# Optimization experiments

Measured on AMD Instinct MI355X. Metric: run time of the kernel, lower is better.

Reference implementation:

```python
import jax, jax.numpy as jnp
import numpy as np

NUM_HEADS = 8

def _proj(x, W, b):
    # 1x1 conv == channel-wise linear: x [B,Ci,H,W], W [Co,Ci], b [Co]
    return jnp.einsum('oi,bihw->bohw', W, x) + b[None, :, None, None]

def setup_inputs() -> dict:
    key = jax.random.key(0)
    ks = jax.random.split(key, 8)
    B, Cin, Cout, H, W = 4, 256, 256, 48, 48
    s = 1.0 / np.sqrt(Cin).astype(np.float32)
    return {
        'queries': jax.random.normal(ks[0], (B, Cin, H, W), jnp.float32),
        'keys':    jax.random.normal(ks[1], (B, Cin, H, W), jnp.float32),
        'values':  jax.random.normal(ks[2], (B, Cin, H, W), jnp.float32),
        'Wq': jax.random.normal(ks[3], (Cout, Cin), jnp.float32) * s,
        'bq': jnp.zeros((Cout,), jnp.float32),
        'Wk': jax.random.normal(ks[4], (Cout, Cin), jnp.float32) * s,
        'bk': jnp.zeros((Cout,), jnp.float32),
        'Wv': jax.random.normal(ks[5], (Cout, Cin), jnp.float32) * s,
        'bv': jnp.zeros((Cout,), jnp.float32),
        'Wo': jax.random.normal(ks[6], (Cout, Cout), jnp.float32) * s,
        'bo': jnp.zeros((Cout,), jnp.float32),
    }

def reference(queries, keys, values, Wq, bq, Wk, bk, Wv, bv, Wo, bo):
    B, _, H, W = values.shape
    Cout = Wq.shape[0]
    d = Cout // NUM_HEADS
    # project and split heads: [B, heads, d, N]
    q = _proj(queries, Wq, bq).reshape(B, NUM_HEADS, d, H * W)
    k = _proj(keys,    Wk, bk).reshape(B, NUM_HEADS, d, H * W)
    v = _proj(values,  Wv, bv).reshape(B, NUM_HEADS, d, H * W)
    scale = 1.0 / np.sqrt(Cout).astype(np.float32)  # source scales by sqrt(out_channels)
    attn = jax.nn.softmax(jnp.einsum('bhdn,bhdm->bhnm', q, k) * scale, axis=-1)
    out = jnp.einsum('bhdm,bhnm->bhdn', v, attn).reshape(B, Cout, H, W)
    return _proj(out, Wo, bo)
```

## Files before the change

### kernel.cpp

```cpp
#include <hip/hip_runtime.h>
#include <hip/hip_bf16.h>

#define NTOT 2304
#define CIN  256
#define DHEAD 32

typedef float  f32x4  __attribute__((ext_vector_type(4)));
typedef __bf16 bf16x8 __attribute__((ext_vector_type(8)));
typedef unsigned short u16x8 __attribute__((ext_vector_type(8)));

static __device__ __forceinline__ unsigned short f2bf(float f) {
    unsigned int u = __float_as_uint(f);
    u += 0x7fff + ((u >> 16) & 1);
    return (unsigned short)(u >> 16);
}

static __device__ __forceinline__ unsigned int pk2(float a, float b) {
    unsigned int r;
    asm("v_cvt_pk_bf16_f32 %0, %1, %2" : "=v"(r) : "v"(a), "v"(b));
    return r;
}

union U8 { unsigned short s[8]; bf16x8 v; };
union PB { unsigned int u[4]; bf16x8 v; };

__global__ __launch_bounds__(256) void pack_weights_kernel(
    const float* __restrict__ Wq, const float* __restrict__ bq,
    const float* __restrict__ Wk, const float* __restrict__ Wv,
    const float* __restrict__ Wo,
    unsigned short* __restrict__ Wq_b, unsigned short* __restrict__ Wk_b,
    unsigned short* __restrict__ Wv_b, unsigned short* __restrict__ Wo_b,
    float* __restrict__ bq_s)
{
    const float SQ = 1.44269504088896340736f / 16.0f;
    int i = blockIdx.x * 256 + threadIdx.x;
    Wq_b[i] = f2bf(Wq[i] * SQ);
    Wk_b[i] = f2bf(Wk[i]);
    Wv_b[i] = f2bf(Wv[i]);
    Wo_b[i] = f2bf(Wo[i]);
    if (blockIdx.x == 0) bq_s[threadIdx.x] = bq[threadIdx.x] * SQ;
}

__global__ __launch_bounds__(256) void proj_all_kernel(
    const float* __restrict__ qx, const float* __restrict__ kx,
    const float* __restrict__ vx,
    const unsigned short* __restrict__ Wqb, const unsigned short* __restrict__ Wkb,
    const unsigned short* __restrict__ Wvb,
    const float* __restrict__ bqs, const float* __restrict__ bk,
    const float* __restrict__ bv,
    unsigned short* __restrict__ Qa, unsigned short* __restrict__ Ka,
    unsigned short* __restrict__ Vp)
{
    const int which = blockIdx.z >> 2;
    const int b     = blockIdx.z & 3;
    const float* x = (which == 0) ? qx : (which == 1) ? kx : vx;
    const unsigned short* Wb = (which == 0) ? Wqb : (which == 1) ? Wkb : Wvb;
    const float* bias = (which == 0) ? bqs : (which == 1) ? bk : bv;
    unsigned short* out = (which == 0) ? Qa : (which == 1) ? Ka : Vp;

    const int n0  = blockIdx.x * 64;
    const int co0 = blockIdx.y * 64;
    const int t = threadIdx.x;
    const int lane = t & 63, w = t >> 6;
    const int g = lane >> 4, l15 = lane & 15;
    const int n_off  = (w & 1) * 32;
    const int co_off = (w >> 1) * 32;

    f32x4 acc[2][2] = {};
    const float* xb = x + (size_t)b * CIN * NTOT;

    for (int ci0 = 0; ci0 < CIN; ci0 += 32) {
        bf16x8 aF[2], bF[2];
        #pragma unroll
        for (int rn = 0; rn < 2; rn++) {
            const float* xp = xb + (size_t)(ci0 + 8 * g) * NTOT + (n0 + n_off + 16 * rn + l15);
            U8 a;
            #pragma unroll
            for (int j = 0; j < 8; j++) a.s[j] = f2bf(xp[(size_t)j * NTOT]);
            aF[rn] = a.v;
        }
        #pragma unroll
        for (int rc = 0; rc < 2; rc++)
            bF[rc] = *reinterpret_cast<const bf16x8*>(
                Wb + (size_t)(co0 + co_off + 16 * rc + l15) * CIN + ci0 + 8 * g);
        #pragma unroll
        for (int rn = 0; rn < 2; rn++)
            #pragma unroll
            for (int rc = 0; rc < 2; rc++)
                acc[rn][rc] = __builtin_amdgcn_mfma_f32_16x16x32_bf16(aF[rn], bF[rc], acc[rn][rc], 0, 0, 0);
    }

    #pragma unroll
    for (int rn = 0; rn < 2; rn++)
    #pragma unroll
    for (int rc = 0; rc < 2; rc++) {
        int co = co0 + co_off + 16 * rc + l15;
        float bs = bias[co];
        int bh = b * 8 + (co >> 5);
        int dd = co & 31;
        int nb = n0 + n_off + 16 * rn + 4 * g;
        if (which == 2) {
            ushort4 v;
            v.x = f2bf(acc[rn][rc][0] + bs);
            v.y = f2bf(acc[rn][rc][1] + bs);
            v.z = f2bf(acc[rn][rc][2] + bs);
            v.w = f2bf(acc[rn][rc][3] + bs);
            int p32 = 8 * ((nb >> 2) & 3) + 4 * ((nb >> 4) & 1);
            *reinterpret_cast<ushort4*>(
                out + (size_t)bh * 73728 + (nb >> 5) * 1024 + dd * 32 + p32) = v;
        } else {
            #pragma unroll
            for (int reg = 0; reg < 4; reg++)
                out[((size_t)bh * NTOT + (nb + reg)) * DHEAD + dd] = f2bf(acc[rn][rc][reg] + bs);
        }
    }
}

__global__ __launch_bounds__(256) void attn_kernel(
    const unsigned short* __restrict__ Qa,
    const unsigned short* __restrict__ Ka,
    const unsigned short* __restrict__ Vp,
    unsigned short* __restrict__ Ot)
{
    __shared__ __align__(16) float olds_a[3][64][17];
    __shared__ __align__(16) float olds_b[3][64][17];
    __shared__ float plsum_a[3][64][3];
    __shared__ float plsum_b[3][64][3];
    __shared__ __align__(16) unsigned short tlds[32][40];
    const int f = blockIdx.x;
    const int c = f & 7;
    const int k = f >> 3;
    const int kq = k / 36;
    const int bh = 4 * c + kq;
    const int qt = k - kq * 36;
    const int b = bh >> 3, h = bh & 7;
    const int t = threadIdx.x;
    const int w = t >> 6, lane = t & 63;
    const int g = lane >> 4, l15 = lane & 15;
    const int n_w = qt * 64;
    const int kw0 = w * 576;

    const unsigned short* Kb  = Ka + (size_t)bh * NTOT * DHEAD + l15 * DHEAD + 8 * g;
    const unsigned short* Vb0 = Vp + (size_t)bh * 73728 + l15 * 32 + 8 * g;
    const unsigned short* Vb1 = Vb0 + 512;

    bf16x8 qBa[2], qBb[2];
    #pragma unroll
    for (int r = 0; r < 2; r++) {
        qBa[r] = *reinterpret_cast<const bf16x8*>(
            Qa + ((size_t)bh * NTOT + n_w + 16 * r + l15) * DHEAD + 8 * g);
        qBb[r] = *reinterpret_cast<const bf16x8*>(
            Qa + ((size_t)bh * NTOT + n_w + 32 + 16 * r + l15) * DHEAD + 8 * g);
    }

    f32x4 oacc_a[2][2] = {};
    f32x4 oacc_b[2][2] = {};
    float psum_a[2] = {0.f, 0.f};
    float psum_b[2] = {0.f, 0.f};
    const f32x4 z4 = {0.f, 0.f, 0.f, 0.f};

    bf16x8 kA[4], kN[4], vA[4], vN[4];
    #pragma unroll
    for (int mc = 0; mc < 4; mc++) {
        kA[mc] = *reinterpret_cast<const bf16x8*>(Kb + (size_t)(kw0 + 16 * mc) * DHEAD);
        kN[mc] = *reinterpret_cast<const bf16x8*>(Kb + (size_t)(kw0 + 64 + 16 * mc) * DHEAD);
    }
    vA[0] = *reinterpret_cast<const bf16x8*>(Vb0 + (size_t)kw0 * 32);
    vA[1] = *reinterpret_cast<const bf16x8*>(Vb0 + (size_t)kw0 * 32 + 1024);
    vA[2] = *reinterpret_cast<const bf16x8*>(Vb1 + (size_t)kw0 * 32);
    vA[3] = *reinterpret_cast<const bf16x8*>(Vb1 + (size_t)kw0 * 32 + 1024);
    vN[0] = *reinterpret_cast<const bf16x8*>(Vb0 + (size_t)(kw0 + 64) * 32);
    vN[1] = *reinterpret_cast<const bf16x8*>(Vb0 + (size_t)(kw0 + 64) * 32 + 1024);
    vN[2] = *reinterpret_cast<const bf16x8*>(Vb1 + (size_t)(kw0 + 64) * 32);
    vN[3] = *reinterpret_cast<const bf16x8*>(Vb1 + (size_t)(kw0 + 64) * 32 + 1024);

    for (int it = 0; it < 9; it++) {
        {
            f32x4 s[2][4];
            #pragma unroll
            for (int r = 0; r < 2; r++)
                #pragma unroll
                for (int mc = 0; mc < 4; mc++)
                    s[r][mc] = __builtin_amdgcn_mfma_f32_16x16x32_bf16(kA[mc], qBa[r], z4, 0, 0, 0);

            float p[2][4][4];
            #pragma unroll
            for (int r = 0; r < 2; r++) {
                #pragma unroll
                for (int mc = 0; mc < 4; mc++)
                    #pragma unroll
                    for (int reg = 0; reg < 4; reg++)
                        p[r][mc][reg] = __builtin_amdgcn_exp2f(s[r][mc][reg]);
                float t0 = (p[r][0][0] + p[r][0][1]) + (p[r][0][2] + p[r][0][3]);
                float t1 = (p[r][1][0] + p[r][1][1]) + (p[r][1][2] + p[r][1][3]);
                float t2 = (p[r][2][0] + p[r][2][1]) + (p[r][2][2] + p[r][2][3]);
                float t3 = (p[r][3][0] + p[r][3][1]) + (p[r][3][2] + p[r][3][3]);
                psum_a[r] += (t0 + t1) + (t2 + t3);
            }

            PB pb[2][2];
            #pragma unroll
            for (int r = 0; r < 2; r++)
                #pragma unroll
                for (int hh = 0; hh < 2; hh++) {
                    pb[r][hh].u[0] = pk2(p[r][2*hh][0],   p[r][2*hh][1]);
                    pb[r][hh].u[1] = pk2(p[r][2*hh][2],   p[r][2*hh][3]);
                    pb[r][hh].u[2] = pk2(p[r][2*hh+1][0], p[r][2*hh+1][1]);
                    pb[r][hh].u[3] = pk2(p[r][2*hh+1][2], p[r][2*hh+1][3]);
                }

            #pragma unroll
            for (int r = 0; r < 2; r++) {
                oacc_a[r][0] = __builtin_amdgcn_mfma_f32_16x16x32_bf16(vA[0], pb[r][0].v, oacc_a[r][0], 0, 0, 0);
                oacc_a[r][0] = __builtin_amdgcn_mfma_f32_16x16x32_bf16(vA[1], pb[r][1].v, oacc_a[r][0], 0, 0, 0);
                oacc_a[r][1] = __builtin_amdgcn_mfma_f32_16x16x32_bf16(vA[2], pb[r][0].v, oacc_a[r][1], 0, 0, 0);
                oacc_a[r][1] = __builtin_amdgcn_mfma_f32_16x16x32_bf16(vA[3], pb[r][1].v, oacc_a[r][1], 0, 0, 0);
            }
        }
        {
            f32x4 s[2][4];
            #pragma unroll
            for (int r = 0; r < 2; r++)
                #pragma unroll
                for (int mc = 0; mc < 4; mc++)
                    s[r][mc] = __builtin_amdgcn_mfma_f32_16x16x32_bf16(kA[mc], qBb[r], z4, 0, 0, 0);

            float p[2][4][4];
            #pragma unroll
            for (int r = 0; r < 2; r++) {
                #pragma unroll
                for (int mc = 0; mc < 4; mc++)
                    #pragma unroll
                    for (int reg = 0; reg < 4; reg++)
                        p[r][mc][reg] = __builtin_amdgcn_exp2f(s[r][mc][reg]);
                float t0 = (p[r][0][0] + p[r][0][1]) + (p[r][0][2] + p[r][0][3]);
                float t1 = (p[r][1][0] + p[r][1][1]) + (p[r][1][2] + p[r][1][3]);
                float t2 = (p[r][2][0] + p[r][2][1]) + (p[r][2][2] + p[r][2][3]);
                float t3 = (p[r][3][0] + p[r][3][1]) + (p[r][3][2] + p[r][3][3]);
                psum_b[r] += (t0 + t1) + (t2 + t3);
            }

            PB pb[2][2];
            #pragma unroll
            for (int r = 0; r < 2; r++)
                #pragma unroll
                for (int hh = 0; hh < 2; hh++) {
                    pb[r][hh].u[0] = pk2(p[r][2*hh][0],   p[r][2*hh][1]);
                    pb[r][hh].u[1] = pk2(p[r][2*hh][2],   p[r][2*hh][3]);
                    pb[r][hh].u[2] = pk2(p[r][2*hh+1][0], p[r][2*hh+1][1]);
                    pb[r][hh].u[3] = pk2(p[r][2*hh+1][2], p[r][2*hh+1][3]);
                }

            #pragma unroll
            for (int r = 0; r < 2; r++) {
                oacc_b[r][0] = __builtin_amdgcn_mfma_f32_16x16x32_bf16(vA[0], pb[r][0].v, oacc_b[r][0], 0, 0, 0);
                oacc_b[r][0] = __builtin_amdgcn_mfma_f32_16x16x32_bf16(vA[1], pb[r][1].v, oacc_b[r][0], 0, 0, 0);
                oacc_b[r][1] = __builtin_amdgcn_mfma_f32_16x16x32_bf16(vA[2], pb[r][0].v, oacc_b[r][1], 0, 0, 0);
                oacc_b[r][1] = __builtin_amdgcn_mfma_f32_16x16x32_bf16(vA[3], pb[r][1].v, oacc_b[r][1], 0, 0, 0);
            }
        }

        int m2 = kw0 + (it + 2) * 64;
        if (it >= 7) m2 = kw0;
        #pragma unroll
        for (int mc = 0; mc < 4; mc++) {
            kA[mc] = kN[mc];
            kN[mc] = *reinterpret_cast<const bf16x8*>(Kb + (size_t)(m2 + 16 * mc) * DHEAD);
        }
        vA[0] = vN[0]; vA[1] = vN[1]; vA[2] = vN[2]; vA[3] = vN[3];
        vN[0] = *reinterpret_cast<const bf16x8*>(Vb0 + (size_t)m2 * 32);
        vN[1] = *reinterpret_cast<const bf16x8*>(Vb0 + (size_t)m2 * 32 + 1024);
        vN[2] = *reinterpret_cast<const bf16x8*>(Vb1 + (size_t)m2 * 32);
        vN[3] = *reinterpret_cast<const bf16x8*>(Vb1 + (size_t)m2 * 32 + 1024);
    }

    if (w > 0) {
        #pragma unroll
        for (int r = 0; r < 2; r++)
            #pragma unroll
            for (int dc = 0; dc < 2; dc++) {
                *reinterpret_cast<f32x4*>(&olds_a[w - 1][lane][8 * r + 4 * dc]) = oacc_a[r][dc];
                *reinterpret_cast<f32x4*>(&olds_b[w - 1][lane][8 * r + 4 * dc]) = oacc_b[r][dc];
            }
        plsum_a[w - 1][lane][0] = psum_a[0];
        plsum_a[w - 1][lane][1] = psum_a[1];
        plsum_b[w - 1][lane][0] = psum_b[0];
        plsum_b[w - 1][lane][1] = psum_b[1];
    }
    __syncthreads();
    if (w == 0) {
        #pragma unroll
        for (int ww = 0; ww < 3; ww++) {
            #pragma unroll
            for (int r = 0; r < 2; r++)
                #pragma unroll
                for (int dc = 0; dc < 2; dc++)
                    oacc_a[r][dc] += *reinterpret_cast<const f32x4*>(&olds_a[ww][lane][8 * r + 4 * dc]);
            psum_a[0] += plsum_a[ww][lane][0];
            psum_a[1] += plsum_a[ww][lane][1];
        }
        float lra[2];
        #pragma unroll
        for (int r = 0; r < 2; r++) {
            float ps = psum_a[r];
            ps += __shfl_xor(ps, 16);
            ps += __shfl_xor(ps, 32);
            lra[r] = 1.0f / ps;
        }
        #pragma unroll
        for (int r = 0; r < 2; r++)
            #pragma unroll
            for (int dc = 0; dc < 2; dc++) {
                ushort4 v;
                v.x = f2bf(oacc_a[r][dc][0] * lra[r]);
                v.y = f2bf(oacc_a[r][dc][1] * lra[r]);
                v.z = f2bf(oacc_a[r][dc][2] * lra[r]);
                v.w = f2bf(oacc_a[r][dc][3] * lra[r]);
                *reinterpret_cast<ushort4*>(&tlds[16 * r + l15][16 * dc + 4 * g]) = v;
            }
        #pragma unroll
        for (int i = 0; i < 2; i++) {
            int row = 16 * i + (lane >> 2), seg = lane & 3;
            u16x8 val = *reinterpret_cast<const u16x8*>(&tlds[row][seg * 8]);
            *reinterpret_cast<u16x8*>(
                Ot + ((size_t)b * NTOT + n_w + row) * CIN + h * DHEAD + seg * 8) = val;
        }

        #pragma unroll
        for (int ww = 0; ww < 3; ww++) {
            #pragma unroll
            for (int r = 0; r < 2; r++)
                #pragma unroll
                for (int dc = 0; dc < 2; dc++)
                    oacc_b[r][dc] += *reinterpret_cast<const f32x4*>(&olds_b[ww][lane][8 * r + 4 * dc]);
            psum_b[0] += plsum_b[ww][lane][0];
            psum_b[1] += plsum_b[ww][lane][1];
        }
        float lrb[2];
        #pragma unroll
        for (int r = 0; r < 2; r++) {
            float ps = psum_b[r];
            ps += __shfl_xor(ps, 16);
            ps += __shfl_xor(ps, 32);
            lrb[r] = 1.0f / ps;
        }
        #pragma unroll
        for (int r = 0; r < 2; r++)
            #pragma unroll
            for (int dc = 0; dc < 2; dc++) {
                ushort4 v;
                v.x = f2bf(oacc_b[r][dc][0] * lrb[r]);
                v.y = f2bf(oacc_b[r][dc][1] * lrb[r]);
                v.z = f2bf(oacc_b[r][dc][2] * lrb[r]);
                v.w = f2bf(oacc_b[r][dc][3] * lrb[r]);
                *reinterpret_cast<ushort4*>(&tlds[16 * r + l15][16 * dc + 4 * g]) = v;
            }
        #pragma unroll
        for (int i = 0; i < 2; i++) {
            int row = 16 * i + (lane >> 2), seg = lane & 3;
            u16x8 val = *reinterpret_cast<const u16x8*>(&tlds[row][seg * 8]);
            *reinterpret_cast<u16x8*>(
                Ot + ((size_t)b * NTOT + n_w + 32 + row) * CIN + h * DHEAD + seg * 8) = val;
        }
    }
}

__global__ __launch_bounds__(256) void out_proj_kernel(
    const unsigned short* __restrict__ Ot,
    const unsigned short* __restrict__ Wob,
    const float* __restrict__ bo,
    float* __restrict__ out)
{
    const int b   = blockIdx.z;
    const int n0  = blockIdx.x * 64;
    const int co0 = blockIdx.y * 64;
    const int t = threadIdx.x;
    const int lane = t & 63, w = t >> 6;
    const int g = lane >> 4, l15 = lane & 15;
    const int n_off  = (w & 1) * 32;
    const int co_off = (w >> 1) * 32;

    f32x4 acc[2][2] = {};
    for (int ci0 = 0; ci0 < CIN; ci0 += 32) {
        bf16x8 aF[2], bF[2];
        #pragma unroll
        for (int rn = 0; rn < 2; rn++)
            aF[rn] = *reinterpret_cast<const bf16x8*>(
                Ot + ((size_t)b * NTOT + n0 + n_off + 16 * rn + l15) * CIN + ci0 + 8 * g);
        #pragma unroll
        for (int rc = 0; rc < 2; rc++)
            bF[rc] = *reinterpret_cast<const bf16x8*>(
                Wob + (size_t)(co0 + co_off + 16 * rc + l15) * CIN + ci0 + 8 * g);
        #pragma unroll
        for (int rn = 0; rn < 2; rn++)
            #pragma unroll
            for (int rc = 0; rc < 2; rc++)
                acc[rn][rc] = __builtin_amdgcn_mfma_f32_16x16x32_bf16(aF[rn], bF[rc], acc[rn][rc], 0, 0, 0);
    }

    #pragma unroll
    for (int rn = 0; rn < 2; rn++)
    #pragma unroll
    for (int rc = 0; rc < 2; rc++) {
        int co = co0 + co_off + 16 * rc + l15;
        float bias = bo[co];
        int nb = n0 + n_off + 16 * rn + 4 * g;
        float4 v;
        v.x = acc[rn][rc][0] + bias;
        v.y = acc[rn][rc][1] + bias;
        v.z = acc[rn][rc][2] + bias;
        v.w = acc[rn][rc][3] + bias;
        *reinterpret_cast<float4*>(out + ((size_t)b * CIN + co) * NTOT + nb) = v;
    }
}

extern "C" void kernel_launch(void* const* d_in, const int* in_sizes, int n_in,
                              void* d_out, int out_size, void* d_ws, size_t ws_size,
                              hipStream_t stream) {
    const float* qx = (const float*)d_in[0];
    const float* kx = (const float*)d_in[1];
    const float* vx = (const float*)d_in[2];
    const float* Wq = (const float*)d_in[3];
    const float* bq = (const float*)d_in[4];
    const float* Wk = (const float*)d_in[5];
    const float* bk = (const float*)d_in[6];
    const float* Wv = (const float*)d_in[7];
    const float* bv = (const float*)d_in[8];
    const float* Wo = (const float*)d_in[9];
    const float* bo = (const float*)d_in[10];
    float* out = (float*)d_out;

    char* ws = (char*)d_ws;
    unsigned short* Wq_b = (unsigned short*)(ws + 0);
    unsigned short* Wk_b = (unsigned short*)(ws + 131072);
    unsigned short* Wv_b = (unsigned short*)(ws + 262144);
    unsigned short* Wo_b = (unsigned short*)(ws + 393216);
    float*          bq_s = (float*)(ws + 524288);
    unsigned short* Qa   = (unsigned short*)(ws + 525312);
    unsigned short* Ka   = (unsigned short*)(ws + 525312 + 1 * 4718592);
    unsigned short* Vp   = (unsigned short*)(ws + 525312 + 2 * 4718592);
    unsigned short* Ot   = (unsigned short*)(ws + 525312 + 3 * 4718592);

    pack_weights_kernel<<<256, 256, 0, stream>>>(Wq, bq, Wk, Wv, Wo,
                                                 Wq_b, Wk_b, Wv_b, Wo_b, bq_s);
    proj_all_kernel<<<dim3(36, 4, 12), 256, 0, stream>>>(
        qx, kx, vx, Wq_b, Wk_b, Wv_b, bq_s, bk, bv, Qa, Ka, Vp);
    attn_kernel<<<dim3(1152), 256, 0, stream>>>(Qa, Ka, Vp, Ot);
    out_proj_kernel<<<dim3(36, 4, 4), 256, 0, stream>>>(Ot, Wo_b, bo, out);
}
```

Measured before the change: 92.62 us.

## Stage projection input tiles through double-buffered LDS with vectorized loads

The projection kernel used to read x straight from global memory with scalar strided loads, one element per channel per lane. It now loads 32x64 fp32 tiles into a padded, double-buffered shared-memory array using float4 loads, prefetching the next channel chunk while the current one is consumed. The goal is coalesced, wider global reads and overlap of loads with MFMA work. In exchange it adds a barrier per step, LDS use that may lower occupancy, and scalar LDS stores.

```diff
diff --git a/kernel.cpp b/kernel.cpp
--- a/kernel.cpp
+++ b/kernel.cpp
@@ -51,6 +51,7 @@
     unsigned short* __restrict__ Qa, unsigned short* __restrict__ Ka,
     unsigned short* __restrict__ Vp)
 {
+    __shared__ float xs[2][32][65];
     const int which = blockIdx.z >> 2;
     const int b     = blockIdx.z & 3;
     const float* x = (which == 0) ? qx : (which == 1) ? kx : vx;
@@ -67,16 +68,43 @@
     const int co_off = (w >> 1) * 32;
 
     f32x4 acc[2][2] = {};
-    const float* xb = x + (size_t)b * CIN * NTOT;
-
-    for (int ci0 = 0; ci0 < CIN; ci0 += 32) {
+    const float* xb = x + (size_t)b * CIN * NTOT + n0;
+
+    const int sci = t >> 3;
+    const int sn  = (t & 7) * 8;
+
+    {
+        const float* src = xb + (size_t)sci * NTOT + sn;
+        float4 va = *reinterpret_cast<const float4*>(src);
+        float4 vb = *reinterpret_cast<const float4*>(src + 4);
+        xs[0][sci][sn + 0] = va.x; xs[0][sci][sn + 1] = va.y;
+        xs[0][sci][sn + 2] = va.z; xs[0][sci][sn + 3] = va.w;
+        xs[0][sci][sn + 4] = vb.x; xs[0][sci][sn + 5] = vb.y;
+        xs[0][sci][sn + 6] = vb.z; xs[0][sci][sn + 7] = vb.w;
+    }
+
+    for (int s = 0; s < 8; s++) {
+        __syncthreads();
+        const int cur = s & 1;
+        if (s < 7) {
+            const float* src = xb + (size_t)((s + 1) * 32 + sci) * NTOT + sn;
+            float4 va = *reinterpret_cast<const float4*>(src);
+            float4 vb = *reinterpret_cast<const float4*>(src + 4);
+            const int nb2 = cur ^ 1;
+            xs[nb2][sci][sn + 0] = va.x; xs[nb2][sci][sn + 1] = va.y;
+            xs[nb2][sci][sn + 2] = va.z; xs[nb2][sci][sn + 3] = va.w;
+            xs[nb2][sci][sn + 4] = vb.x; xs[nb2][sci][sn + 5] = vb.y;
+            xs[nb2][sci][sn + 6] = vb.z; xs[nb2][sci][sn + 7] = vb.w;
+        }
+
+        const int ci0 = s * 32;
         bf16x8 aF[2], bF[2];
         #pragma unroll
         for (int rn = 0; rn < 2; rn++) {
-            const float* xp = xb + (size_t)(ci0 + 8 * g) * NTOT + (n0 + n_off + 16 * rn + l15);
             U8 a;
             #pragma unroll
-            for (int j = 0; j < 8; j++) a.s[j] = f2bf(xp[(size_t)j * NTOT]);
+            for (int j = 0; j < 8; j++)
+                a.s[j] = f2bf(xs[cur][8 * g + j][n_off + 16 * rn + l15]);
             aF[rn] = a.v;
         }
         #pragma unroll
```

Measured after the change: 91.08 us. About the same (-1.7%).
